# Performance work log

Measured on AMD Instinct MI355X. Metric: run time of the kernel, lower is better.

Reference implementation:

```python
import jax, jax.numpy as jnp
import numpy as np

BATCH, SEQ, HIDDEN = 4096, 200, 64


def setup_inputs() -> dict:
    key = jax.random.key(0)
    ks = jax.random.split(key, 7)
    s = 1.0 / np.sqrt(HIDDEN)  # torch LSTM default init scale
    return {
        "inputs": jax.random.normal(ks[0], (BATCH, SEQ, 1), dtype=jnp.float32),
        "W_ih": jax.random.uniform(ks[1], (4 * HIDDEN, 1), jnp.float32, -s, s),
        "W_hh": jax.random.uniform(ks[2], (4 * HIDDEN, HIDDEN), jnp.float32, -s, s),
        "b_ih": jax.random.uniform(ks[3], (4 * HIDDEN,), jnp.float32, -s, s),
        "b_hh": jax.random.uniform(ks[4], (4 * HIDDEN,), jnp.float32, -s, s),
        "W_lin": jax.random.uniform(ks[5], (1, SEQ * HIDDEN), jnp.float32, -s, s),
        "b_lin": jax.random.uniform(ks[6], (1,), jnp.float32, -s, s),
    }


def _lstm(inputs, W_ih, W_hh, b_ih, b_hh):
    # inputs: [B, T, 1] (batch_first). Precompute input projections for all t.
    B, T, _ = inputs.shape
    H = W_hh.shape[1]
    # [T, B, 4H]
    x_proj = jnp.einsum('bti,gi->tbg', inputs, W_ih) + (b_ih + b_hh)

    def step(carry, xg):
        h, c = carry
        gates = xg + h @ W_hh.T  # [B, 4H]
        i, f, g, o = jnp.split(gates, 4, axis=-1)
        i = jax.nn.sigmoid(i)
        f = jax.nn.sigmoid(f)
        g = jnp.tanh(g)
        o = jax.nn.sigmoid(o)
        c = f * c + i * g
        h = o * jnp.tanh(c)
        return (h, c), h

    h0 = jnp.zeros((B, H), dtype=inputs.dtype)
    c0 = jnp.zeros((B, H), dtype=inputs.dtype)
    _, hs = jax.lax.scan(step, (h0, c0), x_proj)  # hs: [T, B, H]
    return jnp.transpose(hs, (1, 0, 2))  # [B, T, H]


def reference(inputs, W_ih, W_hh, b_ih, b_hh, W_lin, b_lin):
    hs = _lstm(inputs, W_ih, W_hh, b_ih, b_hh)          # [B, T, H]
    flat = hs.reshape(hs.shape[0], -1)                   # [B, T*H]
    return flat @ W_lin.T + b_lin                        # [B, 1]
```

## Files before the change

kernel.cpp:

```cpp
#include <hip/hip_runtime.h>

#define SEQ 200
#define HID 64
#define BT  8
#define NBLK (4096 / BT)

typedef _Float16 f16;
typedef _Float16 f16x8 __attribute__((ext_vector_type(8)));
typedef float    f32x4 __attribute__((ext_vector_type(4)));

#define LOG2E 1.44269504088896340736f

#if __has_builtin(__builtin_amdgcn_exp2f)
#define EXP2F(x) __builtin_amdgcn_exp2f(x)
#else
#define EXP2F(x) __expf(0.69314718056f * (x))
#endif
#define RCPF(x) __builtin_amdgcn_rcpf(x)

__global__ __launch_bounds__(256, 2)
void qlstm_v14(const float* __restrict__ x,
               const float* __restrict__ W_ih,
               const float* __restrict__ W_hh,
               const float* __restrict__ b_ih,
               const float* __restrict__ b_hh,
               const float* __restrict__ W_lin,
               const float* __restrict__ b_lin,
               float* __restrict__ out)
{
    __shared__ float x_lds[BT][201];
    __shared__ f16   h_frag[2][16 * HID];
    __shared__ float wl_lds[SEQ * HID];
    __shared__ float out_part[4][BT];

    const int tid = threadIdx.x;
    const int w   = tid >> 6;
    const int l   = tid & 63;
    const int m   = l & 15;
    const int a   = l >> 4;
    const int b0  = blockIdx.x * BT;

    const float qs[4] = {LOG2E, LOG2E, 2.0f * LOG2E, LOG2E};

    for (int i = tid; i < BT * SEQ; i += 256) {
        int b = i / SEQ, t = i - b * SEQ;
        x_lds[b][t] = x[(size_t)b0 * SEQ + i];
    }
    {
        const float4* src = (const float4*)W_lin;
        float4* dst = (float4*)wl_lds;
        for (int i = tid; i < SEQ * HID / 4; i += 256) dst[i] = src[i];
    }
    for (int i = tid; i < 1024; i += 256) ((float*)h_frag)[i] = 0.0f;

    f16x8 Bf[4][2];
    float wihq[4], biasq[4];
    #pragma unroll
    for (int q = 0; q < 4; ++q) {
        const int n = q * 64 + w * 16 + m;
        wihq[q]  = W_ih[n] * qs[q];
        biasq[q] = (b_ih[n] + b_hh[n]) * qs[q];
        #pragma unroll
        for (int kk = 0; kk < 2; ++kk) {
            const float4* p = (const float4*)(W_hh + n * HID + kk * 32 + a * 8);
            float4 lo = p[0], hi = p[1];
            f16x8 f;
            f[0] = (f16)(lo.x * qs[q]); f[1] = (f16)(lo.y * qs[q]);
            f[2] = (f16)(lo.z * qs[q]); f[3] = (f16)(lo.w * qs[q]);
            f[4] = (f16)(hi.x * qs[q]); f[5] = (f16)(hi.y * qs[q]);
            f[6] = (f16)(hi.z * qs[q]); f[7] = (f16)(hi.w * qs[q]);
            Bf[q][kk] = f;
        }
    }

    const int jpw = w * 16 + m;
    const int ra0 = m * 128 + (((0 + a) ^ (m & 7)) << 4);
    const int ra1 = m * 128 + (((4 + a) ^ (m & 7)) << 4);
    const int bA = 2 * a;
    const int bB = 2 * a + 1;
    const int R0 = 4 * a, R1 = 4 * a + 1;
    const int hwA = R0 * 128 + (((jpw >> 3) ^ (R0 & 7)) << 4) + (jpw & 7) * 2;
    const int hwB = R1 * 128 + (((jpw >> 3) ^ (R1 & 7)) << 4) + (jpw & 7) * 2;

    const char* hbytes = (const char*)h_frag;

    float cA = 0.0f, cB = 0.0f, oA = 0.0f, oB = 0.0f;
    const float t2s = 2.0f * LOG2E;

    __syncthreads();

    for (int t = 0; t < SEQ; ++t) {
        const int rb = (t & 1) << 11;
        const int wb = rb ^ 2048;

        __builtin_amdgcn_s_setprio(1);
        const f16x8 A0 = *(const f16x8*)(hbytes + rb + ra0);
        const f16x8 A1 = *(const f16x8*)(hbytes + rb + ra1);
        const float x0 = x_lds[bA][t];
        const float x1 = x_lds[bB][t];
        const float wl = wl_lds[t * HID + jpw];

        f32x4 acc[4];
        #pragma unroll
        for (int q = 0; q < 4; ++q) {
            const float i0 = fmaf(x0, wihq[q], biasq[q]);
            const float i1 = fmaf(x1, wihq[q], biasq[q]);
            f32x4 ini;
            ini[0] = i0; ini[1] = i1; ini[2] = i0; ini[3] = i1;
            f32x4 z = __builtin_amdgcn_mfma_f32_16x16x32_f16(A0, Bf[q][0], ini, 0, 0, 0);
            acc[q]  = __builtin_amdgcn_mfma_f32_16x16x32_f16(A1, Bf[q][1], z, 0, 0, 0);
        }
        __builtin_amdgcn_s_setprio(0);

        {
            const float eA = EXP2F(-acc[0][0]);
            const float eC = EXP2F(-acc[1][0]);
            const float eB = EXP2F(acc[2][0]);
            const float eE = EXP2F(-acc[3][0]);
            const float ig = (eB - 1.0f) * RCPF((1.0f + eA) * (eB + 1.0f));
            const float gf = RCPF(1.0f + eC);
            cA = fmaf(gf, cA, t2s * ig);
            const float eD = EXP2F(cA);
            const float h  = (eD - 1.0f) * RCPF((1.0f + eE) * (eD + 1.0f));
            *(f16*)((char*)h_frag + wb + hwA) = (f16)h;
            oA = fmaf(h, wl, oA);
        }
        {
            const float eA = EXP2F(-acc[0][1]);
            const float eC = EXP2F(-acc[1][1]);
            const float eB = EXP2F(acc[2][1]);
            const float eE = EXP2F(-acc[3][1]);
            const float ig = (eB - 1.0f) * RCPF((1.0f + eA) * (eB + 1.0f));
            const float gf = RCPF(1.0f + eC);
            cB = fmaf(gf, cB, t2s * ig);
            const float eD = EXP2F(cB);
            const float h  = (eD - 1.0f) * RCPF((1.0f + eE) * (eD + 1.0f));
            *(f16*)((char*)h_frag + wb + hwB) = (f16)h;
            oB = fmaf(h, wl, oB);
        }

        __syncthreads();
    }

    float vA = oA, vB = oB;
    #pragma unroll
    for (int off = 1; off < 16; off <<= 1) {
        vA += __shfl_xor(vA, off, 64);
        vB += __shfl_xor(vB, off, 64);
    }
    if (m == 0) {
        out_part[w][bA] = vA;
        out_part[w][bB] = vB;
    }
    __syncthreads();
    if (tid < BT) {
        out[b0 + tid] = out_part[0][tid] + out_part[1][tid]
                      + out_part[2][tid] + out_part[3][tid] + b_lin[0];
    }
}

extern "C" void kernel_launch(void* const* d_in, const int* in_sizes, int n_in,
                              void* d_out, int out_size, void* d_ws, size_t ws_size,
                              hipStream_t stream) {
    const float* x     = (const float*)d_in[0];
    const float* W_ih  = (const float*)d_in[1];
    const float* W_hh  = (const float*)d_in[2];
    const float* b_ih  = (const float*)d_in[3];
    const float* b_hh  = (const float*)d_in[4];
    const float* W_lin = (const float*)d_in[5];
    const float* b_lin = (const float*)d_in[6];
    float* out = (float*)d_out;

    dim3 grid(NBLK);
    dim3 block(256);
    qlstm_v14<<<grid, block, 0, stream>>>(x, W_ih, W_hh, b_ih, b_hh,
                                          W_lin, b_lin, out);
}
```

Baseline: 84.51 us.

## Interleave two independent batch groups per block to overlap MFMA with activations

Each block now handles 16 batch rows split into two independent groups with separate double-buffered hidden-state tiles. The loop is software-pipelined so that one group's MFMA gate computation runs while the other group's transcendental activation and cell update execute, hiding the serial dependency latency within each timestep. This halves the grid and lowers launch bounds to one block per CU, giving up cross-block occupancy in exchange for explicit intra-wave overlap. It also keeps more live state in registers.

```diff
diff --git a/kernel.cpp b/kernel.cpp
--- a/kernel.cpp
+++ b/kernel.cpp
@@ -2,7 +2,7 @@
 
 #define SEQ 200
 #define HID 64
-#define BT  8
+#define BT  16
 #define NBLK (4096 / BT)
 
 typedef _Float16 f16;
@@ -18,8 +18,8 @@
 #endif
 #define RCPF(x) __builtin_amdgcn_rcpf(x)
 
-__global__ __launch_bounds__(256, 2)
-void qlstm_v14(const float* __restrict__ x,
+__global__ __launch_bounds__(256, 1)
+void qlstm_v17(const float* __restrict__ x,
                const float* __restrict__ W_ih,
                const float* __restrict__ W_hh,
                const float* __restrict__ b_ih,
@@ -29,7 +29,7 @@
                float* __restrict__ out)
 {
     __shared__ float x_lds[BT][201];
-    __shared__ f16   h_frag[2][16 * HID];
+    __shared__ f16   h_frag[2][2][16 * HID];
     __shared__ float wl_lds[SEQ * HID];
     __shared__ float out_part[4][BT];
 
@@ -51,7 +51,7 @@
         float4* dst = (float4*)wl_lds;
         for (int i = tid; i < SEQ * HID / 4; i += 256) dst[i] = src[i];
     }
-    for (int i = tid; i < 1024; i += 256) ((float*)h_frag)[i] = 0.0f;
+    for (int i = tid; i < 2048; i += 256) ((float*)h_frag)[i] = 0.0f;
 
     f16x8 Bf[4][2];
     float wihq[4], biasq[4];
@@ -76,81 +76,175 @@
     const int jpw = w * 16 + m;
     const int ra0 = m * 128 + (((0 + a) ^ (m & 7)) << 4);
     const int ra1 = m * 128 + (((4 + a) ^ (m & 7)) << 4);
-    const int bA = 2 * a;
-    const int bB = 2 * a + 1;
     const int R0 = 4 * a, R1 = 4 * a + 1;
     const int hwA = R0 * 128 + (((jpw >> 3) ^ (R0 & 7)) << 4) + (jpw & 7) * 2;
     const int hwB = R1 * 128 + (((jpw >> 3) ^ (R1 & 7)) << 4) + (jpw & 7) * 2;
 
-    const char* hbytes = (const char*)h_frag;
-
-    float cA = 0.0f, cB = 0.0f, oA = 0.0f, oB = 0.0f;
+    const int r0A = 2 * a,     r0B = 2 * a + 1;
+    const int r1A = 8 + 2 * a, r1B = 8 + 2 * a + 1;
+
+    const char* hb = (const char*)h_frag;
+
+    float c0A = 0.f, c0B = 0.f, c1A = 0.f, c1B = 0.f;
+    float o0A = 0.f, o0B = 0.f, o1A = 0.f, o1B = 0.f;
     const float t2s = 2.0f * LOG2E;
 
-    __syncthreads();
-
-    for (int t = 0; t < SEQ; ++t) {
-        const int rb = (t & 1) << 11;
-        const int wb = rb ^ 2048;
-
-        __builtin_amdgcn_s_setprio(1);
-        const f16x8 A0 = *(const f16x8*)(hbytes + rb + ra0);
-        const f16x8 A1 = *(const f16x8*)(hbytes + rb + ra1);
-        const float x0 = x_lds[bA][t];
-        const float x1 = x_lds[bB][t];
-        const float wl = wl_lds[t * HID + jpw];
-
-        f32x4 acc[4];
+    f32x4 acc0[4], acc1[4];
+
+    auto GATE = [&](f32x4 (&acc)[4], const int rbyte, const float xa, const float xb) {
+        const f16x8 A0 = *(const f16x8*)(hb + rbyte + ra0);
+        const f16x8 A1 = *(const f16x8*)(hb + rbyte + ra1);
         #pragma unroll
         for (int q = 0; q < 4; ++q) {
-            const float i0 = fmaf(x0, wihq[q], biasq[q]);
-            const float i1 = fmaf(x1, wihq[q], biasq[q]);
+            const float i0 = fmaf(xa, wihq[q], biasq[q]);
+            const float i1 = fmaf(xb, wihq[q], biasq[q]);
             f32x4 ini;
             ini[0] = i0; ini[1] = i1; ini[2] = i0; ini[3] = i1;
             f32x4 z = __builtin_amdgcn_mfma_f32_16x16x32_f16(A0, Bf[q][0], ini, 0, 0, 0);
             acc[q]  = __builtin_amdgcn_mfma_f32_16x16x32_f16(A1, Bf[q][1], z, 0, 0, 0);
         }
-        __builtin_amdgcn_s_setprio(0);
-
-        {
-            const float eA = EXP2F(-acc[0][0]);
-            const float eC = EXP2F(-acc[1][0]);
-            const float eB = EXP2F(acc[2][0]);
-            const float eE = EXP2F(-acc[3][0]);
-            const float ig = (eB - 1.0f) * RCPF((1.0f + eA) * (eB + 1.0f));
-            const float gf = RCPF(1.0f + eC);
-            cA = fmaf(gf, cA, t2s * ig);
-            const float eD = EXP2F(cA);
-            const float h  = (eD - 1.0f) * RCPF((1.0f + eE) * (eD + 1.0f));
-            *(f16*)((char*)h_frag + wb + hwA) = (f16)h;
-            oA = fmaf(h, wl, oA);
-        }
-        {
-            const float eA = EXP2F(-acc[0][1]);
-            const float eC = EXP2F(-acc[1][1]);
-            const float eB = EXP2F(acc[2][1]);
-            const float eE = EXP2F(-acc[3][1]);
-            const float ig = (eB - 1.0f) * RCPF((1.0f + eA) * (eB + 1.0f));
-            const float gf = RCPF(1.0f + eC);
-            cB = fmaf(gf, cB, t2s * ig);
-            const float eD = EXP2F(cB);
-            const float h  = (eD - 1.0f) * RCPF((1.0f + eE) * (eD + 1.0f));
-            *(f16*)((char*)h_frag + wb + hwB) = (f16)h;
-            oB = fmaf(h, wl, oB);
-        }
+    };
+
+    __syncthreads();
+
+    GATE(acc0, 0, x_lds[r0A][0], x_lds[r0B][0]);
+
+    for (int t = 0; t < SEQ - 1; ++t) {
+        const int p  = t & 1;
+        const int pn = p ^ 1;
+        const float wl = wl_lds[t * HID + jpw];
 
         __syncthreads();
-    }
-
-    float vA = oA, vB = oB;
+
+        GATE(acc1, 4096 + p * 2048, x_lds[r1A][t], x_lds[r1B][t]);
+        {
+            const float eA = EXP2F(-acc0[0][0]);
+            const float eC = EXP2F(-acc0[1][0]);
+            const float eB = EXP2F(acc0[2][0]);
+            const float eE = EXP2F(-acc0[3][0]);
+            const float ig = (eB - 1.0f) * RCPF((1.0f + eA) * (eB + 1.0f));
+            const float gf = RCPF(1.0f + eC);
+            c0A = fmaf(gf, c0A, t2s * ig);
+            const float eD = EXP2F(c0A);
+            const float h  = (eD - 1.0f) * RCPF((1.0f + eE) * (eD + 1.0f));
+            *(f16*)((char*)h_frag + pn * 2048 + hwA) = (f16)h;
+            o0A = fmaf(h, wl, o0A);
+        }
+        {
+            const float eA = EXP2F(-acc0[0][1]);
+            const float eC = EXP2F(-acc0[1][1]);
+            const float eB = EXP2F(acc0[2][1]);
+            const float eE = EXP2F(-acc0[3][1]);
+            const float ig = (eB - 1.0f) * RCPF((1.0f + eA) * (eB + 1.0f));
+            const float gf = RCPF(1.0f + eC);
+            c0B = fmaf(gf, c0B, t2s * ig);
+            const float eD = EXP2F(c0B);
+            const float h  = (eD - 1.0f) * RCPF((1.0f + eE) * (eD + 1.0f));
+            *(f16*)((char*)h_frag + pn * 2048 + hwB) = (f16)h;
+            o0B = fmaf(h, wl, o0B);
+        }
+
+        __syncthreads();
+
+        GATE(acc0, pn * 2048, x_lds[r0A][t + 1], x_lds[r0B][t + 1]);
+        {
+            const float eA = EXP2F(-acc1[0][0]);
+            const float eC = EXP2F(-acc1[1][0]);
+            const float eB = EXP2F(acc1[2][0]);
+            const float eE = EXP2F(-acc1[3][0]);
+            const float ig = (eB - 1.0f) * RCPF((1.0f + eA) * (eB + 1.0f));
+            const float gf = RCPF(1.0f + eC);
+            c1A = fmaf(gf, c1A, t2s * ig);
+            const float eD = EXP2F(c1A);
+            const float h  = (eD - 1.0f) * RCPF((1.0f + eE) * (eD + 1.0f));
+            *(f16*)((char*)h_frag + 4096 + pn * 2048 + hwA) = (f16)h;
+            o1A = fmaf(h, wl, o1A);
+        }
+        {
+            const float eA = EXP2F(-acc1[0][1]);
+            const float eC = EXP2F(-acc1[1][1]);
+            const float eB = EXP2F(acc1[2][1]);
+            const float eE = EXP2F(-acc1[3][1]);
+            const float ig = (eB - 1.0f) * RCPF((1.0f + eA) * (eB + 1.0f));
+            const float gf = RCPF(1.0f + eC);
+            c1B = fmaf(gf, c1B, t2s * ig);
+            const float eD = EXP2F(c1B);
+            const float h  = (eD - 1.0f) * RCPF((1.0f + eE) * (eD + 1.0f));
+            *(f16*)((char*)h_frag + 4096 + pn * 2048 + hwB) = (f16)h;
+            o1B = fmaf(h, wl, o1B);
+        }
+    }
+
+    {
+        const int t = SEQ - 1;
+        const int p = t & 1;
+        const float wl = wl_lds[t * HID + jpw];
+
+        __syncthreads();
+        GATE(acc1, 4096 + p * 2048, x_lds[r1A][t], x_lds[r1B][t]);
+        {
+            const float eA = EXP2F(-acc0[0][0]);
+            const float eC = EXP2F(-acc0[1][0]);
+            const float eB = EXP2F(acc0[2][0]);
+            const float eE = EXP2F(-acc0[3][0]);
+            const float ig = (eB - 1.0f) * RCPF((1.0f + eA) * (eB + 1.0f));
+            const float gf = RCPF(1.0f + eC);
+            c0A = fmaf(gf, c0A, t2s * ig);
+            const float eD = EXP2F(c0A);
+            const float h  = (eD - 1.0f) * RCPF((1.0f + eE) * (eD + 1.0f));
+            o0A = fmaf(h, wl, o0A);
+        }
+        {
+            const float eA = EXP2F(-acc0[0][1]);
+            const float eC = EXP2F(-acc0[1][1]);
+            const float eB = EXP2F(acc0[2][1]);
+            const float eE = EXP2F(-acc0[3][1]);
+            const float ig = (eB - 1.0f) * RCPF((1.0f + eA) * (eB + 1.0f));
+            const float gf = RCPF(1.0f + eC);
+            c0B = fmaf(gf, c0B, t2s * ig);
+            const float eD = EXP2F(c0B);
+            const float h  = (eD - 1.0f) * RCPF((1.0f + eE) * (eD + 1.0f));
+            o0B = fmaf(h, wl, o0B);
+        }
+        {
+            const float eA = EXP2F(-acc1[0][0]);
+            const float eC = EXP2F(-acc1[1][0]);
+            const float eB = EXP2F(acc1[2][0]);
+            const float eE = EXP2F(-acc1[3][0]);
+            const float ig = (eB - 1.0f) * RCPF((1.0f + eA) * (eB + 1.0f));
+            const float gf = RCPF(1.0f + eC);
+            c1A = fmaf(gf, c1A, t2s * ig);
+            const float eD = EXP2F(c1A);
+            const float h  = (eD - 1.0f) * RCPF((1.0f + eE) * (eD + 1.0f));
+            o1A = fmaf(h, wl, o1A);
+        }
+        {
+            const float eA = EXP2F(-acc1[0][1]);
+            const float eC = EXP2F(-acc1[1][1]);
+            const float eB = EXP2F(acc1[2][1]);
+            const float eE = EXP2F(-acc1[3][1]);
+            const float ig = (eB - 1.0f) * RCPF((1.0f + eA) * (eB + 1.0f));
+            const float gf = RCPF(1.0f + eC);
+            c1B = fmaf(gf, c1B, t2s * ig);
+            const float eD = EXP2F(c1B);
+            const float h  = (eD - 1.0f) * RCPF((1.0f + eE) * (eD + 1.0f));
+            o1B = fmaf(h, wl, o1B);
+        }
+    }
+
+    float v0A = o0A, v0B = o0B, v1A = o1A, v1B = o1B;
     #pragma unroll
     for (int off = 1; off < 16; off <<= 1) {
-        vA += __shfl_xor(vA, off, 64);
-        vB += __shfl_xor(vB, off, 64);
+        v0A += __shfl_xor(v0A, off, 64);
+        v0B += __shfl_xor(v0B, off, 64);
+        v1A += __shfl_xor(v1A, off, 64);
+        v1B += __shfl_xor(v1B, off, 64);
     }
     if (m == 0) {
-        out_part[w][bA] = vA;
-        out_part[w][bB] = vB;
+        out_part[w][r0A] = v0A;
+        out_part[w][r0B] = v0B;
+        out_part[w][r1A] = v1A;
+        out_part[w][r1B] = v1B;
     }
     __syncthreads();
     if (tid < BT) {
@@ -173,6 +267,6 @@
 
     dim3 grid(NBLK);
     dim3 block(256);
-    qlstm_v14<<<grid, block, 0, stream>>>(x, W_ih, W_hh, b_ih, b_hh,
+    qlstm_v17<<<grid, block, 0, stream>>>(x, W_ih, W_hh, b_ih, b_hh,
                                           W_lin, b_lin, out);
 }
```

New measurement: 136.8 us. 61.9% more time.
